# Optimization experiments

Hardware: AMD Instinct MI355X
Metric: run time of the kernel (lower is better)

Reference implementation:

```python
import jax, jax.numpy as jnp
import numpy as np

B, N, F = 2, 2048, 64
H, C = 4, 32          # attention heads, channels per head
HID = 128             # hidden_size
HIN = H * C           # hidden_size_in = 128
MASK = -10e9          # spektral dense-GAT mask constant


def setup_inputs() -> dict:
    key = jax.random.key(0)
    ks = jax.random.split(key, 48)
    inp = {}
    inp['x'] = jax.random.normal(ks[0], (B, N, F), dtype=jnp.float32)
    adj = (jax.random.uniform(ks[1], (B, N, N)) < 0.03).astype(jnp.float32)
    inp['a'] = jnp.clip(adj + jnp.eye(N, dtype=jnp.float32)[None], 0.0, 1.0)
    inp['h_p'] = jax.random.normal(ks[2], (B, N, HID), dtype=jnp.float32) * 0.1
    inp['h_mu'] = jax.random.normal(ks[3], (B, N, HID), dtype=jnp.float32) * 0.1
    inp['h_sigma'] = jax.random.normal(ks[4], (B, N, HID), dtype=jnp.float32) * 0.1
    # GAT params
    inp['gat_kernel'] = jax.random.normal(ks[5], (F, H, C), dtype=jnp.float32) / np.float32(np.sqrt(F))
    inp['gat_attn_self'] = jax.random.normal(ks[6], (H, C), dtype=jnp.float32) * 0.1
    inp['gat_attn_neigh'] = jax.random.normal(ks[7], (H, C), dtype=jnp.float32) * 0.1
    inp['gat_bias'] = jnp.zeros((H * C,), dtype=jnp.float32)
    # GRU-style gate params for p / mu / sigma
    ki = 8
    for nm in ('p', 'mu', 'sigma'):
        for g in ('u', 'r', 'c'):
            inp[f'W_{g}_{nm}'] = jax.random.normal(ks[ki], (HID + HIN, HID), dtype=jnp.float32) / np.float32(np.sqrt(HID + HIN)); ki += 1
            inp[f'b_{g}_{nm}'] = jax.random.normal(ks[ki], (N, 1), dtype=jnp.float32) * 0.05; ki += 1
    # bilinear decoders
    for nm in ('p', 'mu', 'sigma'):
        inp[f'R_{nm}'] = jax.random.normal(ks[ki], (HID, HID), dtype=jnp.float32) / np.float32(np.sqrt(HID)); ki += 1
    return inp


def _gat(x, a, kernel, attn_self, attn_neigh, bias):
    # dense spektral GATConv, concat_heads=True, no activation
    h = jnp.einsum('bnf,fhc->bnhc', x, kernel)                 # [B,N,H,C]
    s_self = jnp.einsum('bnhc,hc->bnh', h, attn_self)          # [B,N,H]
    s_neigh = jnp.einsum('bnhc,hc->bnh', h, attn_neigh)        # [B,N,H]
    scores = s_self[:, :, None, :] + s_neigh[:, None, :, :]    # [B,N,N,H]
    scores = jax.nn.leaky_relu(scores, negative_slope=0.2)
    scores = scores + MASK * (1.0 - a)[..., None]
    attn = jax.nn.softmax(scores, axis=2)                      # softmax over neighbors j
    out = jnp.einsum('bijh,bjhc->bihc', attn, h)               # [B,N,H,C]
    return out.reshape(out.shape[0], out.shape[1], H * C) + bias


def _gru(conv, h, Wu, Wr, Wc, bu, br, bc):
    ch = jnp.concatenate([conv, h], axis=-1)                   # [B,N,HIN+HID]
    u = jax.nn.sigmoid(bu + ch @ Wu)                           # bias [N,1] broadcasts
    r = jax.nn.sigmoid(br + ch @ Wr)
    c = jnp.tanh(bc + jnp.concatenate([conv, r * h], axis=-1) @ Wc)
    return u * h + (1.0 - u) * c


def _bilinear(h, R):
    return jnp.einsum('bnh,hk,bmk->bnm', h, R, h)              # x R x^T


def reference(x, a, h_p, h_mu, h_sigma,
              gat_kernel, gat_attn_self, gat_attn_neigh, gat_bias,
              W_u_p, b_u_p, W_r_p, b_r_p, W_c_p, b_c_p,
              W_u_mu, b_u_mu, W_r_mu, b_r_mu, W_c_mu, b_c_mu,
              W_u_sigma, b_u_sigma, W_r_sigma, b_r_sigma, W_c_sigma, b_c_sigma,
              R_p, R_mu, R_sigma):
    conv = _gat(x, a, gat_kernel, gat_attn_self, gat_attn_neigh, gat_bias)
    hp = _gru(conv, h_p, W_u_p, W_r_p, W_c_p, b_u_p, b_r_p, b_c_p)
    hmu = _gru(conv, h_mu, W_u_mu, W_r_mu, W_c_mu, b_u_mu, b_r_mu, b_c_mu)
    hsg = _gru(conv, h_sigma, W_u_sigma, W_r_sigma, W_c_sigma, b_u_sigma, b_r_sigma, b_c_sigma)
    p = _bilinear(hp, R_p)
    mu = _bilinear(hmu, R_mu)
    sigma = _bilinear(hsg, R_sigma)
    logits = jnp.stack([p, mu, sigma], axis=-1)                # [B,N,N,3]
    return logits, hp, hmu, hsg
```

## Files before the change

kernel.cpp:

```cpp
#include <hip/hip_runtime.h>
#include <hip/hip_bf16.h>

typedef __attribute__((ext_vector_type(4))) float f32x4;
typedef __attribute__((ext_vector_type(8))) short bf16x8;

static constexpr int B   = 2;
static constexpr int N   = 2048;
static constexpr int F   = 64;
static constexpr int H   = 4;
static constexpr int HID = 128;
static constexpr int BN  = B * N;
static constexpr size_t LOG_SZ = (size_t)B * N * N * 3;

__device__ __forceinline__ float sigmoidf_(float x) { return 1.0f / (1.0f + __expf(-x)); }
__device__ __forceinline__ float tanhf_(float x) {
  float e = __expf(2.0f * x);
  return 1.0f - 2.0f / (e + 1.0f);
}
__device__ __forceinline__ void split_bf16(float v, short& hi, short& lo) {
  unsigned u = __float_as_uint(v);
  unsigned hr = (u + 0x7FFFu + ((u >> 16) & 1u)) >> 16;
  hi = (short)hr;
  float hv = __uint_as_float(hr << 16);
  float res = v - hv;
  unsigned u2 = __float_as_uint(res);
  lo = (short)((u2 + 0x7FFFu + ((u2 >> 16) & 1u)) >> 16);
}

__device__ __forceinline__ void stage16(const short* gp, short* lp) {
  __builtin_amdgcn_global_load_lds(
      (const __attribute__((address_space(1))) void*)gp,
      (__attribute__((address_space(3))) void*)lp, 16, 0, 0);
}

struct PreArgs {
  const float* x; const float* gk; const float* asel; const float* anei;
  float* hfeat; float* sself; float* sneigh;
  const float* h[3];
  short* hh[3]; short* hl[3];
  const float* src[12];
  short* whi[12]; short* wlo[12];
  int nks[12];
};
__global__ __launch_bounds__(256) void k_pre(PreArgs pa) {
  const int bid = blockIdx.x;
  if (bid < BN / 2) {
    const int t = threadIdx.x;
    const int r = t >> 7, tt = t & 127;
    const int bn = bid * 2 + r;
    __shared__ float xs[2][F];
    if (tt < F) xs[r][tt] = pa.x[(size_t)bn * F + tt];
    const size_t o = (size_t)bn * HID + tt;
    { short hi, lo; split_bf16(pa.h[0][o], hi, lo); pa.hh[0][o] = hi; pa.hl[0][o] = lo; }
    { short hi, lo; split_bf16(pa.h[1][o], hi, lo); pa.hh[1][o] = hi; pa.hl[1][o] = lo; }
    { short hi, lo; split_bf16(pa.h[2][o], hi, lo); pa.hh[2][o] = hi; pa.hl[2][o] = lo; }
    __syncthreads();
    float acc = 0.f;
    #pragma unroll 8
    for (int f = 0; f < F; ++f) acc += xs[r][f] * pa.gk[f * HID + tt];
    pa.hfeat[o] = acc;
    float ps = acc * pa.asel[tt];
    float pn = acc * pa.anei[tt];
    #pragma unroll
    for (int d = 16; d >= 1; d >>= 1) {
      ps += __shfl_xor(ps, d, 32);
      pn += __shfl_xor(pn, d, 32);
    }
    if ((tt & 31) == 0) {
      pa.sself [bn * H + (tt >> 5)] = ps;
      pa.sneigh[bn * H + (tt >> 5)] = pn;
    }
  } else {
    const int pb = bid - BN / 2;
    const int m = pb >> 3, cf = pb & 7;
    const int nksv = pa.nks[m];
    const int wv = threadIdx.x >> 6, lane = threadIdx.x & 63;
    const float* src = pa.src[m];
    short* ph = pa.whi[m];
    short* pl = pa.wlo[m];
    const int col = cf * 16 + (lane & 15);
    const int krow = (lane >> 4) * 8;
    for (int ks = wv; ks < nksv; ks += 4) {
      bf16x8 vh, vl;
      #pragma unroll
      for (int e = 0; e < 8; ++e) {
        const int k = ks * 32 + krow + e;
        short hi, lo; split_bf16(src[(size_t)k * HID + col], hi, lo);
        vh[e] = hi; vl[e] = lo;
      }
      const size_t o = (((size_t)cf * nksv + ks) * 64 + lane) * 8;
      *(bf16x8*)&ph[o] = vh;
      *(bf16x8*)&pl[o] = vl;
    }
  }
}

__global__ __launch_bounds__(256) void k_attn(
    const float* __restrict__ a, const float* __restrict__ hfeat,
    const float* __restrict__ sself, const float* __restrict__ sneigh,
    const float* __restrict__ bias,
    short* __restrict__ conv_hi, short* __restrict__ conv_lo) {
  const int wv   = threadIdx.x >> 6;
  const int lane = threadIdx.x & 63;
  const int bi   = blockIdx.x * 4 + wv;
  const int bbase = bi & ~(N - 1);
  __shared__ int   nbr[4][256];
  __shared__ float wts[4][256][4];
  int*   nb       = nbr[wv];
  float (*wt)[4]  = wts[wv];

  const float si0 = sself[bi * H + 0];
  const float si1 = sself[bi * H + 1];
  const float si2 = sself[bi * H + 2];
  const float si3 = sself[bi * H + 3];
  float den0 = 0.f, den1 = 0.f, den2 = 0.f, den3 = 0.f;
  float acc0 = 0.f, acc1 = 0.f;
  const unsigned long long lmlt = ((unsigned long long)1 << lane) - 1ull;
  const float* arow = a + (size_t)bi * N;
  const float* hb   = hfeat + (size_t)bbase * HID;
  const float* snb  = sneigh + (size_t)bbase * H;
  const int h0 = lane >> 5;
  int num = 0;

  auto flush = [&]() {
    asm volatile("s_waitcnt lgkmcnt(0)" ::: "memory");
    for (int n = lane; n < num; n += 64) {
      const int j = nb[n];
      f32x4 sn = *(const f32x4*)&snb[(size_t)j * H];
      float s0 = si0 + sn[0]; s0 = (s0 > 0.f) ? s0 : 0.2f * s0;
      float s1 = si1 + sn[1]; s1 = (s1 > 0.f) ? s1 : 0.2f * s1;
      float s2 = si2 + sn[2]; s2 = (s2 > 0.f) ? s2 : 0.2f * s2;
      float s3 = si3 + sn[3]; s3 = (s3 > 0.f) ? s3 : 0.2f * s3;
      float w0 = __expf(s0), w1 = __expf(s1), w2 = __expf(s2), w3 = __expf(s3);
      wt[n][0] = w0; wt[n][1] = w1; wt[n][2] = w2; wt[n][3] = w3;
      den0 += w0; den1 += w1; den2 += w2; den3 += w3;
    }
    asm volatile("s_waitcnt lgkmcnt(0)" ::: "memory");
    #pragma unroll 4
    for (int n = 0; n < num; ++n) {
      const int j  = nb[n];
      const float wA = wt[n][h0];
      const float wB = wt[n][h0 + 2];
      const float* hr = hb + (size_t)j * HID;
      acc0 += wA * hr[lane];
      acc1 += wB * hr[lane + 64];
    }
    asm volatile("s_waitcnt lgkmcnt(0)" ::: "memory");
    num = 0;
  };

  for (int jb = 0; jb < N; jb += 256) {
    f32x4 av = *(const f32x4*)&arow[jb + lane * 4];
    #pragma unroll
    for (int e = 0; e < 4; ++e) {
      const unsigned long long m = __ballot(av[e] > 0.5f);
      if (av[e] > 0.5f) {
        const int pos = num + __popcll(m & lmlt);
        nb[pos] = jb + lane * 4 + e;
      }
      num += __popcll(m);
      if (num > 192) flush();
    }
  }
  if (num > 0) flush();

  #pragma unroll
  for (int d = 32; d >= 1; d >>= 1) {
    den0 += __shfl_xor(den0, d, 64);
    den1 += __shfl_xor(den1, d, 64);
    den2 += __shfl_xor(den2, d, 64);
    den3 += __shfl_xor(den3, d, 64);
  }
  const float dA = h0 ? den1 : den0;
  const float dB = h0 ? den3 : den2;
  const float v0 = acc0 / dA + bias[lane];
  const float v1 = acc1 / dB + bias[64 + lane];
  { short hi, lo; split_bf16(v0, hi, lo);
    conv_hi[(size_t)bi * HID + lane] = hi; conv_lo[(size_t)bi * HID + lane] = lo; }
  { short hi, lo; split_bf16(v1, hi, lo);
    conv_hi[(size_t)bi * HID + 64 + lane] = hi; conv_lo[(size_t)bi * HID + 64 + lane] = lo; }
}

struct GArgs {
  const short* chi; const short* clo;
  const float* h[3];
  const short* hhi[3]; const short* hlo[3];
  const float* bu[3]; const float* br[3]; const float* bc[3];
  const short* WuH[3]; const short* WuL[3];
  const short* WrH[3]; const short* WrL[3];
  const short* WcH[3]; const short* WcL[3];
  const short* RtH[3]; const short* RtL[3];
  float* u_ws[3];
  short* rhh[3]; short* rhl[3];
  short* hph[3]; short* hpl[3];
  float* hout[3]; __hip_bfloat16* hb[3]; __hip_bfloat16* gb[3];
};

__global__ __launch_bounds__(256) void k_ur(GArgs ga) {
  const int wv = threadIdx.x >> 6, lane = threadIdx.x & 63;
  const int bx = blockIdx.x, cg = blockIdx.y;
  const int gate = blockIdx.z & 1, cell = blockIdx.z >> 1;
  const int lr = lane & 15, lg = lane >> 4, kb = lg * 8;
  const int R0 = bx * 64 + wv * 16;
  __shared__ short wlds[2][16][64][8];

  bf16x8 a_h[8], a_l[8];
  {
    const size_t ab = (size_t)(R0 + lr) * HID + kb;
    const short* hhi = ga.hhi[cell]; const short* hlo = ga.hlo[cell];
    #pragma unroll
    for (int ks = 0; ks < 4; ++ks) {
      a_h[ks]     = *(const bf16x8*)&ga.chi[ab + ks * 32];
      a_l[ks]     = *(const bf16x8*)&ga.clo[ab + ks * 32];
      a_h[4 + ks] = *(const bf16x8*)&hhi[ab + ks * 32];
      a_l[4 + ks] = *(const bf16x8*)&hlo[ab + ks * 32];
    }
  }
  {
    const short* WH = gate ? ga.WrH[cell] : ga.WuH[cell];
    const short* WL = gate ? ga.WrL[cell] : ga.WuL[cell];
    #pragma unroll
    for (int i = 0; i < 8; ++i) {
      const int fid = wv * 8 + i;
      const int combo = fid >> 4, f = fid & 15;
      const short* src = combo ? WL : WH;
      const short* gp = src + (((size_t)((cg * 2 + (f >> 3)) * 8 + (f & 7))) * 64 + lane) * 8;
      stage16(gp, &wlds[combo][f][0][0]);
    }
  }
  asm volatile("s_waitcnt vmcnt(0)" ::: "memory");
  __syncthreads();

  f32x4 acc[2] = {};
  #pragma unroll
  for (int ks = 0; ks < 8; ++ks) {
    const bf16x8 ah = a_h[ks], al = a_l[ks];
    #pragma unroll
    for (int cfl = 0; cfl < 2; ++cfl) {
      const int f = cfl * 8 + ks;
      bf16x8 bh = *(const bf16x8*)&wlds[0][f][lane][0];
      bf16x8 bl = *(const bf16x8*)&wlds[1][f][lane][0];
      acc[cfl] = __builtin_amdgcn_mfma_f32_16x16x32_bf16(ah, bh, acc[cfl], 0, 0, 0);
      acc[cfl] = __builtin_amdgcn_mfma_f32_16x16x32_bf16(ah, bl, acc[cfl], 0, 0, 0);
      acc[cfl] = __builtin_amdgcn_mfma_f32_16x16x32_bf16(al, bh, acc[cfl], 0, 0, 0);
    }
  }
  if (gate == 0) {
    const float* bu = ga.bu[cell];
    float* uws = ga.u_ws[cell];
    #pragma unroll
    for (int cfl = 0; cfl < 2; ++cfl) {
      const int col = cg * 32 + cfl * 16 + lr;
      #pragma unroll
      for (int q = 0; q < 4; ++q) {
        const int row = R0 + lg * 4 + q;
        uws[(size_t)row * HID + col] = sigmoidf_(acc[cfl][q] + bu[row & (N - 1)]);
      }
    }
  } else {
    const float* br = ga.br[cell];
    const float* hsrc = ga.h[cell];
    short* rhh = ga.rhh[cell]; short* rhl = ga.rhl[cell];
    #pragma unroll
    for (int cfl = 0; cfl < 2; ++cfl) {
      const int col = cg * 32 + cfl * 16 + lr;
      #pragma unroll
      for (int q = 0; q < 4; ++q) {
        const int row = R0 + lg * 4 + q;
        const float rv = sigmoidf_(acc[cfl][q] + br[row & (N - 1)]);
        const float rhv = rv * hsrc[(size_t)row * HID + col];
        short hi, lo; split_bf16(rhv, hi, lo);
        rhh[(size_t)row * HID + col] = hi;
        rhl[(size_t)row * HID + col] = lo;
      }
    }
  }
}

__global__ __launch_bounds__(256) void k_c(GArgs ga) {
  const int wv = threadIdx.x >> 6, lane = threadIdx.x & 63;
  const int bx = blockIdx.x, cg = blockIdx.y, cell = blockIdx.z;
  const int lr = lane & 15, lg = lane >> 4, kb = lg * 8;
  const int R0 = bx * 64 + wv * 16;
  __shared__ short wlds[2][16][64][8];

  bf16x8 a_h[8], a_l[8];
  {
    const size_t ab = (size_t)(R0 + lr) * HID + kb;
    const short* rhh = ga.rhh[cell]; const short* rhl = ga.rhl[cell];
    #pragma unroll
    for (int ks = 0; ks < 4; ++ks) {
      a_h[ks]     = *(const bf16x8*)&ga.chi[ab + ks * 32];
      a_l[ks]     = *(const bf16x8*)&ga.clo[ab + ks * 32];
      a_h[4 + ks] = *(const bf16x8*)&rhh[ab + ks * 32];
      a_l[4 + ks] = *(const bf16x8*)&rhl[ab + ks * 32];
    }
  }
  {
    const short* WH = ga.WcH[cell];
    const short* WL = ga.WcL[cell];
    #pragma unroll
    for (int i = 0; i < 8; ++i) {
      const int fid = wv * 8 + i;
      const int combo = fid >> 4, f = fid & 15;
      const short* src = combo ? WL : WH;
      const short* gp = src + (((size_t)((cg * 2 + (f >> 3)) * 8 + (f & 7))) * 64 + lane) * 8;
      stage16(gp, &wlds[combo][f][0][0]);
    }
  }
  asm volatile("s_waitcnt vmcnt(0)" ::: "memory");
  __syncthreads();

  f32x4 acc[2] = {};
  #pragma unroll
  for (int ks = 0; ks < 8; ++ks) {
    const bf16x8 ah = a_h[ks], al = a_l[ks];
    #pragma unroll
    for (int cfl = 0; cfl < 2; ++cfl) {
      const int f = cfl * 8 + ks;
      bf16x8 bh = *(const bf16x8*)&wlds[0][f][lane][0];
      bf16x8 bl = *(const bf16x8*)&wlds[1][f][lane][0];
      acc[cfl] = __builtin_amdgcn_mfma_f32_16x16x32_bf16(ah, bh, acc[cfl], 0, 0, 0);
      acc[cfl] = __builtin_amdgcn_mfma_f32_16x16x32_bf16(ah, bl, acc[cfl], 0, 0, 0);
      acc[cfl] = __builtin_amdgcn_mfma_f32_16x16x32_bf16(al, bh, acc[cfl], 0, 0, 0);
    }
  }
  const float* bc = ga.bc[cell];
  const float* uw = ga.u_ws[cell];
  const float* hsrc = ga.h[cell];
  float* hout = ga.hout[cell];
  __hip_bfloat16* hbo = ga.hb[cell];
  short* hph = ga.hph[cell]; short* hpl = ga.hpl[cell];
  #pragma unroll
  for (int cfl = 0; cfl < 2; ++cfl) {
    const int col = cg * 32 + cfl * 16 + lr;
    #pragma unroll
    for (int q = 0; q < 4; ++q) {
      const int row = R0 + lg * 4 + q;
      const float cv = tanhf_(acc[cfl][q] + bc[row & (N - 1)]);
      const float uv = uw[(size_t)row * HID + col];
      const float hv = hsrc[(size_t)row * HID + col];
      const float o = uv * hv + (1.f - uv) * cv;
      hout[(size_t)row * HID + col] = o;
      hbo[(size_t)row * HID + col] = __float2bfloat16(o);
      short hi, lo; split_bf16(o, hi, lo);
      hph[(size_t)row * HID + col] = hi;
      hpl[(size_t)row * HID + col] = lo;
    }
  }
}

__global__ __launch_bounds__(256) void k_g(GArgs ga) {
  const int wv = threadIdx.x >> 6, lane = threadIdx.x & 63;
  const int bx = blockIdx.x, cg = blockIdx.y, cell = blockIdx.z;
  const int lr = lane & 15, lg = lane >> 4, kb = lg * 8;
  const int R0 = bx * 64 + wv * 16;
  __shared__ short wlds[2][8][64][8];

  bf16x8 a_h[4], a_l[4];
  {
    const size_t ab = (size_t)(R0 + lr) * HID + kb;
    const short* hph = ga.hph[cell]; const short* hpl = ga.hpl[cell];
    #pragma unroll
    for (int ks = 0; ks < 4; ++ks) {
      a_h[ks] = *(const bf16x8*)&hph[ab + ks * 32];
      a_l[ks] = *(const bf16x8*)&hpl[ab + ks * 32];
    }
  }
  {
    #pragma unroll
    for (int i = 0; i < 4; ++i) {
      const int fid = wv * 4 + i;
      const int combo = fid >> 3, f = fid & 7;
      const short* src = combo ? ga.RtL[cell] : ga.RtH[cell];
      const short* gp = src + (((size_t)((cg * 2 + (f >> 2)) * 4 + (f & 3))) * 64 + lane) * 8;
      stage16(gp, &wlds[combo][f][0][0]);
    }
  }
  asm volatile("s_waitcnt vmcnt(0)" ::: "memory");
  __syncthreads();

  f32x4 acc[2] = {};
  #pragma unroll
  for (int ks = 0; ks < 4; ++ks) {
    const bf16x8 ah = a_h[ks], al = a_l[ks];
    #pragma unroll
    for (int cfl = 0; cfl < 2; ++cfl) {
      const int f = cfl * 4 + ks;
      bf16x8 bh = *(const bf16x8*)&wlds[0][f][lane][0];
      bf16x8 bl = *(const bf16x8*)&wlds[1][f][lane][0];
      acc[cfl] = __builtin_amdgcn_mfma_f32_16x16x32_bf16(ah, bh, acc[cfl], 0, 0, 0);
      acc[cfl] = __builtin_amdgcn_mfma_f32_16x16x32_bf16(ah, bl, acc[cfl], 0, 0, 0);
      acc[cfl] = __builtin_amdgcn_mfma_f32_16x16x32_bf16(al, bh, acc[cfl], 0, 0, 0);
    }
  }
  __hip_bfloat16* gbo = ga.gb[cell];
  #pragma unroll
  for (int cfl = 0; cfl < 2; ++cfl) {
    const int col = cg * 32 + cfl * 16 + lr;
    #pragma unroll
    for (int q = 0; q < 4; ++q) {
      const int row = R0 + lg * 4 + q;
      gbo[(size_t)row * HID + col] = __float2bfloat16(acc[cfl][q]);
    }
  }
}

__global__ __launch_bounds__(256) void k_bilinear(
    const __hip_bfloat16* __restrict__ g0, const __hip_bfloat16* __restrict__ g1,
    const __hip_bfloat16* __restrict__ g2, const __hip_bfloat16* __restrict__ h0,
    const __hip_bfloat16* __restrict__ h1, const __hip_bfloat16* __restrict__ h2,
    float* __restrict__ out) {
  const int ti = blockIdx.x, tj = blockIdx.y, b = blockIdx.z;
  const int t = threadIdx.x;
  const int w = t >> 6, l = t & 63;
  const int wi = w >> 1, wj = w & 1;
  const int i_base = ti * 64 + wi * 32;
  const int j_base = tj * 64 + wj * 32;
  const __hip_bfloat16* gbs[3] = {g0, g1, g2};
  const __hip_bfloat16* hbs[3] = {h0, h1, h2};
  const int lr = l & 15;
  const int kb = (l >> 4) * 8;
  f32x4 acc[3][2][2] = {};
  for (int k0 = 0; k0 < HID; k0 += 32) {
    bf16x8 af[3][2], bfr[3][2];
    #pragma unroll
    for (int d = 0; d < 3; ++d) {
      #pragma unroll
      for (int m = 0; m < 2; ++m) {
        af[d][m]  = *(const bf16x8*)&gbs[d][(size_t)(b * N + i_base + m * 16 + lr) * HID + k0 + kb];
        bfr[d][m] = *(const bf16x8*)&hbs[d][(size_t)(b * N + j_base + m * 16 + lr) * HID + k0 + kb];
      }
    }
    #pragma unroll
    for (int d = 0; d < 3; ++d)
      #pragma unroll
      for (int mi = 0; mi < 2; ++mi)
        #pragma unroll
        for (int mj = 0; mj < 2; ++mj)
          acc[d][mi][mj] = __builtin_amdgcn_mfma_f32_16x16x32_bf16(
              af[d][mi], bfr[d][mj], acc[d][mi][mj], 0, 0, 0);
  }
  const int orow = (l >> 4) * 4;
  const int col  = l & 15;
  #pragma unroll
  for (int mi = 0; mi < 2; ++mi)
    #pragma unroll
    for (int mj = 0; mj < 2; ++mj)
      #pragma unroll
      for (int r = 0; r < 4; ++r) {
        const int row = i_base + mi * 16 + orow + r;
        const int cc  = j_base + mj * 16 + col;
        float* p = &out[(((size_t)(b * N + row)) * N + cc) * 3];
        p[0] = acc[0][mi][mj][r];
        p[1] = acc[1][mi][mj][r];
        p[2] = acc[2][mi][mj][r];
      }
}

extern "C" void kernel_launch(void* const* d_in, const int* in_sizes, int n_in,
                              void* d_out, int out_size, void* d_ws, size_t ws_size,
                              hipStream_t stream) {
  (void)in_sizes; (void)n_in; (void)out_size; (void)ws_size;
  const float* a    = (const float*)d_in[1];
  const float* bias = (const float*)d_in[8];

  float* ws      = (float*)d_ws;
  float* hfeat   = ws;
  float* sself   = hfeat + (size_t)BN * HID;
  float* sneigh  = sself + (size_t)BN * H;
  float* u_ws0   = sneigh + (size_t)BN * H;
  short* sp      = (short*)(u_ws0 + 3 * (size_t)BN * HID);
  auto alloc_s = [&](size_t n) { short* p = sp; sp += n; return p; };

  short* conv_hi = alloc_s((size_t)BN * HID);
  short* conv_lo = alloc_s((size_t)BN * HID);
  short* h_hi[3]; short* h_lo[3];
  for (int c = 0; c < 3; ++c) { h_hi[c] = alloc_s((size_t)BN * HID); h_lo[c] = alloc_s((size_t)BN * HID); }
  short* rh_hi[3]; short* rh_lo[3];
  for (int c = 0; c < 3; ++c) { rh_hi[c] = alloc_s((size_t)BN * HID); rh_lo[c] = alloc_s((size_t)BN * HID); }
  short* hp_hi[3]; short* hp_lo[3];
  for (int c = 0; c < 3; ++c) { hp_hi[c] = alloc_s((size_t)BN * HID); hp_lo[c] = alloc_s((size_t)BN * HID); }
  __hip_bfloat16* hbb[3]; __hip_bfloat16* gbb[3];
  for (int c = 0; c < 3; ++c) {
    hbb[c] = (__hip_bfloat16*)alloc_s((size_t)BN * HID);
    gbb[c] = (__hip_bfloat16*)alloc_s((size_t)BN * HID);
  }

  float* out = (float*)d_out;

  PreArgs pa;
  pa.x = (const float*)d_in[0];
  pa.gk = (const float*)d_in[5];
  pa.asel = (const float*)d_in[6];
  pa.anei = (const float*)d_in[7];
  pa.hfeat = hfeat; pa.sself = sself; pa.sneigh = sneigh;

  GArgs ga;
  ga.chi = conv_hi; ga.clo = conv_lo;
  ga.h[0] = (const float*)d_in[2];
  ga.h[1] = (const float*)d_in[3];
  ga.h[2] = (const float*)d_in[4];
  for (int c = 0; c < 3; ++c) {
    pa.h[c] = ga.h[c];
    pa.hh[c] = h_hi[c]; pa.hl[c] = h_lo[c];
    const int base = 9 + c * 6;
    ga.hhi[c] = h_hi[c]; ga.hlo[c] = h_lo[c];
    ga.bu[c] = (const float*)d_in[base + 1];
    ga.br[c] = (const float*)d_in[base + 3];
    ga.bc[c] = (const float*)d_in[base + 5];
    short* wu_h = alloc_s(256 * 128); short* wu_l = alloc_s(256 * 128);
    short* wr_h = alloc_s(256 * 128); short* wr_l = alloc_s(256 * 128);
    short* wc_h = alloc_s(256 * 128); short* wc_l = alloc_s(256 * 128);
    short* rt_h = alloc_s(128 * 128); short* rt_l = alloc_s(128 * 128);
    const int pb = c * 4;
    pa.src[pb + 0] = (const float*)d_in[base + 0]; pa.whi[pb + 0] = wu_h; pa.wlo[pb + 0] = wu_l; pa.nks[pb + 0] = 8;
    pa.src[pb + 1] = (const float*)d_in[base + 2]; pa.whi[pb + 1] = wr_h; pa.wlo[pb + 1] = wr_l; pa.nks[pb + 1] = 8;
    pa.src[pb + 2] = (const float*)d_in[base + 4]; pa.whi[pb + 2] = wc_h; pa.wlo[pb + 2] = wc_l; pa.nks[pb + 2] = 8;
    pa.src[pb + 3] = (const float*)d_in[27 + c];   pa.whi[pb + 3] = rt_h; pa.wlo[pb + 3] = rt_l; pa.nks[pb + 3] = 4;
    ga.WuH[c] = wu_h; ga.WuL[c] = wu_l;
    ga.WrH[c] = wr_h; ga.WrL[c] = wr_l;
    ga.WcH[c] = wc_h; ga.WcL[c] = wc_l;
    ga.RtH[c] = rt_h; ga.RtL[c] = rt_l;
    ga.u_ws[c] = u_ws0 + (size_t)c * BN * HID;
    ga.rhh[c] = rh_hi[c]; ga.rhl[c] = rh_lo[c];
    ga.hph[c] = hp_hi[c]; ga.hpl[c] = hp_lo[c];
    ga.hout[c] = out + LOG_SZ + (size_t)c * BN * HID;
    ga.hb[c] = hbb[c];
    ga.gb[c] = gbb[c];
  }

  k_pre<<<BN / 2 + 96, 256, 0, stream>>>(pa);
  k_attn<<<BN / 4, 256, 0, stream>>>(a, hfeat, sself, sneigh, bias, conv_hi, conv_lo);
  k_ur<<<dim3(BN / 64, 4, 6), 256, 0, stream>>>(ga);
  k_c<<<dim3(BN / 64, 4, 3), 256, 0, stream>>>(ga);
  k_g<<<dim3(BN / 64, 4, 3), 256, 0, stream>>>(ga);
  dim3 g2(N / 64, N / 64, B);
  k_bilinear<<<g2, 256, 0, stream>>>(gbb[0], gbb[1], gbb[2],
                                     hbb[0], hbb[1], hbb[2], out);
}
```

Before: 116.3 us.

## Split attention row across four waves and use nontemporal stores for outputs

The GAT attention kernel now assigns one block per node row, with each of the four waves scanning a 512-column slice of the adjacency row. Partial numerators and softmax denominators are reduced through shared memory before the bf16 split is written. The launch grows to four times as many blocks, aiming to raise parallelism and shorten the per-wave serial scan, at the cost of a block barrier and a shared-memory reduction. Stores of the large logits tensor and the hidden outputs become nontemporal so they do not pollute the cache.

```diff
diff --git a/kernel.cpp b/kernel.cpp
--- a/kernel.cpp
+++ b/kernel.cpp
@@ -102,12 +102,14 @@
     short* __restrict__ conv_hi, short* __restrict__ conv_lo) {
   const int wv   = threadIdx.x >> 6;
   const int lane = threadIdx.x & 63;
-  const int bi   = blockIdx.x * 4 + wv;
+  const int bi   = blockIdx.x;
   const int bbase = bi & ~(N - 1);
-  __shared__ int   nbr[4][256];
-  __shared__ float wts[4][256][4];
-  int*   nb       = nbr[wv];
-  float (*wt)[4]  = wts[wv];
+  __shared__ int   nbr[4][128];
+  __shared__ float wts[4][128][4];
+  __shared__ float racc[4][128];
+  __shared__ float rden[4][4];
+  int*   nb      = nbr[wv];
+  float (*wt)[4] = wts[wv];
 
   const float si0 = sself[bi * H + 0];
   const float si1 = sself[bi * H + 1];
@@ -116,10 +118,11 @@
   float den0 = 0.f, den1 = 0.f, den2 = 0.f, den3 = 0.f;
   float acc0 = 0.f, acc1 = 0.f;
   const unsigned long long lmlt = ((unsigned long long)1 << lane) - 1ull;
-  const float* arow = a + (size_t)bi * N;
+  const float* arow = a + (size_t)bi * N + wv * 512;
   const float* hb   = hfeat + (size_t)bbase * HID;
   const float* snb  = sneigh + (size_t)bbase * H;
   const int h0 = lane >> 5;
+  const int jbase0 = wv * 512;
   int num = 0;
 
   auto flush = [&]() {
@@ -149,17 +152,18 @@
     num = 0;
   };
 
-  for (int jb = 0; jb < N; jb += 256) {
+  #pragma unroll
+  for (int jb = 0; jb < 512; jb += 256) {
     f32x4 av = *(const f32x4*)&arow[jb + lane * 4];
     #pragma unroll
     for (int e = 0; e < 4; ++e) {
       const unsigned long long m = __ballot(av[e] > 0.5f);
       if (av[e] > 0.5f) {
         const int pos = num + __popcll(m & lmlt);
-        nb[pos] = jb + lane * 4 + e;
+        nb[pos] = jbase0 + jb + lane * 4 + e;
       }
       num += __popcll(m);
-      if (num > 192) flush();
+      if (num > 64) flush();
     }
   }
   if (num > 0) flush();
@@ -171,14 +175,23 @@
     den2 += __shfl_xor(den2, d, 64);
     den3 += __shfl_xor(den3, d, 64);
   }
-  const float dA = h0 ? den1 : den0;
-  const float dB = h0 ? den3 : den2;
-  const float v0 = acc0 / dA + bias[lane];
-  const float v1 = acc1 / dB + bias[64 + lane];
-  { short hi, lo; split_bf16(v0, hi, lo);
-    conv_hi[(size_t)bi * HID + lane] = hi; conv_lo[(size_t)bi * HID + lane] = lo; }
-  { short hi, lo; split_bf16(v1, hi, lo);
-    conv_hi[(size_t)bi * HID + 64 + lane] = hi; conv_lo[(size_t)bi * HID + 64 + lane] = lo; }
+  racc[wv][lane]      = acc0;
+  racc[wv][lane + 64] = acc1;
+  if (lane == 0) {
+    rden[wv][0] = den0; rden[wv][1] = den1;
+    rden[wv][2] = den2; rden[wv][3] = den3;
+  }
+  __syncthreads();
+  if (threadIdx.x < HID) {
+    const int ch = threadIdx.x;
+    const float tot = racc[0][ch] + racc[1][ch] + racc[2][ch] + racc[3][ch];
+    const int hh = ch >> 5;
+    const float dd = rden[0][hh] + rden[1][hh] + rden[2][hh] + rden[3][hh];
+    const float v = tot / dd + bias[ch];
+    short hi, lo; split_bf16(v, hi, lo);
+    conv_hi[(size_t)bi * HID + ch] = hi;
+    conv_lo[(size_t)bi * HID + ch] = lo;
+  }
 }
 
 struct GArgs {
@@ -341,7 +354,7 @@
       const float uv = uw[(size_t)row * HID + col];
       const float hv = hsrc[(size_t)row * HID + col];
       const float o = uv * hv + (1.f - uv) * cv;
-      hout[(size_t)row * HID + col] = o;
+      __builtin_nontemporal_store(o, &hout[(size_t)row * HID + col]);
       hbo[(size_t)row * HID + col] = __float2bfloat16(o);
       short hi, lo; split_bf16(o, hi, lo);
       hph[(size_t)row * HID + col] = hi;
@@ -452,9 +465,9 @@
         const int row = i_base + mi * 16 + orow + r;
         const int cc  = j_base + mj * 16 + col;
         float* p = &out[(((size_t)(b * N + row)) * N + cc) * 3];
-        p[0] = acc[0][mi][mj][r];
-        p[1] = acc[1][mi][mj][r];
-        p[2] = acc[2][mi][mj][r];
+        __builtin_nontemporal_store(acc[0][mi][mj][r], p + 0);
+        __builtin_nontemporal_store(acc[1][mi][mj][r], p + 1);
+        __builtin_nontemporal_store(acc[2][mi][mj][r], p + 2);
       }
 }
 
@@ -531,7 +544,7 @@
   }
 
   k_pre<<<BN / 2 + 96, 256, 0, stream>>>(pa);
-  k_attn<<<BN / 4, 256, 0, stream>>>(a, hfeat, sself, sneigh, bias, conv_hi, conv_lo);
+  k_attn<<<BN, 256, 0, stream>>>(a, hfeat, sself, sneigh, bias, conv_hi, conv_lo);
   k_ur<<<dim3(BN / 64, 4, 6), 256, 0, stream>>>(ga);
   k_c<<<dim3(BN / 64, 4, 3), 256, 0, stream>>>(ga);
   k_g<<<dim3(BN / 64, 4, 3), 256, 0, stream>>>(ga);
```

After: 115.3 us. About the same (-0.9%).
